# Performance work log

Measured on AMD Instinct MI355X. Metric: run time of the kernel, lower is better.

The kernel has to match this reference:

```python
import jax, jax.numpy as jnp
import numpy as np

R = 0.25
M = 0


def setup_inputs() -> dict:
    key = jax.random.key(0)
    k1, k2, k3, k4 = jax.random.split(key, 4)
    B, T_cmp, C = 2, 4096, 4096
    H, KVH, D, W = 32, 8, 128, 512
    return {
        "x_m": jax.random.normal(k1, (B, 2 * T_cmp, C), dtype=jnp.float32),
        "xm_cmp": jax.random.normal(k2, (B, T_cmp, C), dtype=jnp.float32),
        "q_w": jax.random.normal(k3, (B, H, W, D), dtype=jnp.float32),
        "km_cmp": jax.random.normal(k4, (B, KVH, T_cmp, D), dtype=jnp.float32),
    }


def reference(x_m, xm_cmp, q_w, km_cmp):
    B, T_cmp, C = xm_cmp.shape
    groups = q_w.shape[1] // km_cmp.shape[1]  # GQA repeat factor
    scaling = q_w.shape[-1] ** -0.5

    # importance_score: repeat kv heads, scaled-dot attention, softmax over keys,
    # sum over query positions, mean over heads -> [B, T_cmp]
    km = jnp.repeat(km_cmp, groups, axis=1)  # [B, H, T_cmp, D]
    scores = jnp.einsum('bhqd,bhkd->bhqk', q_w, km) * scaling
    weights = jax.nn.softmax(scores, axis=-1)
    importance = weights.sum(axis=2).mean(axis=1)  # [B, T_cmp]

    # select_indices: static top-k count
    k = min(int(R * T_cmp + M * (1 - R) / 2), T_cmp)
    _, idx = jax.lax.top_k(importance, k)  # [B, k]

    # interleave_selected: selected compressed tokens are replaced by their
    # two original tokens x_m[2t], x_m[2t+1]; others keep xm_cmp[t].
    b_idx = jnp.arange(B)[:, None]
    expand_mask = jnp.zeros((B, T_cmp), dtype=bool).at[b_idx, idx].set(True)
    sizes = jnp.where(expand_mask, 2, 1)
    start = jnp.cumsum(sizes, axis=1) - sizes  # output start position per token
    T_out = T_cmp + k

    first = jnp.where(expand_mask[..., None], x_m[:, ::2], xm_cmp)  # [B,T_cmp,C]
    second = x_m[:, 1::2]  # [B, T_cmp, C]
    pos2 = jnp.where(expand_mask, start + 1, T_out)  # non-expanded -> dummy slot

    y = jnp.zeros((B, T_out + 1, C), dtype=xm_cmp.dtype)
    y = y.at[b_idx, start].set(first)
    y = y.at[b_idx, pos2].set(second)
    return y[:, :T_out]
```

## Files before the change

kernel.cpp:

```cpp
#include <hip/hip_runtime.h>
#include <hip/hip_bf16.h>

#define B_    2
#define H_    32
#define KVH_  8
#define T_    4096
#define C_    4096
#define D_    128
#define W_    512
#define KTOP  1024
#define TOUT  (T_ + KTOP)
#define QB    64
#define NQB   (W_/QB)
#define TB    64
#define NTT   (T_/TB)
#define NPART (H_*NQB)
#define NBLK  (NQB*H_*B_)
#define SCALE 0.08838834764831845f

typedef __attribute__((ext_vector_type(8))) _Float16 half8;
typedef __attribute__((ext_vector_type(4))) float f32x4;

__device__ __forceinline__ void gload16(const void* g, void* l) {
    __builtin_amdgcn_global_load_lds(
        (const __attribute__((address_space(1))) void*)g,
        (__attribute__((address_space(3))) void*)l, 16, 0, 0);
}

__global__ __launch_bounds__(256) void convert_k_kernel(
    const float* __restrict__ km, _Float16* __restrict__ Khw,
    _Float16* __restrict__ Klw)
{
    int g = blockIdx.x*256 + threadIdx.x;
    size_t e = (size_t)g*8;
    int d0 = (int)(e & 127);
    size_t row = e >> 7;
    int t = (int)(row & (T_-1));
    size_t bk = row >> 12;
    int r = t & 63, tt = t >> 6;
    size_t off = (bk<<19) + (size_t)tt*(TB*D_) + (size_t)r*D_ + (d0 ^ ((r&7)<<3));
    float4 v0 = *(const float4*)(km + e);
    float4 v1 = *(const float4*)(km + e + 4);
    float f[8] = {v0.x,v0.y,v0.z,v0.w,v1.x,v1.y,v1.z,v1.w};
    half8 hh, hl;
#pragma unroll
    for (int i = 0; i < 8; ++i) {
        _Float16 hi = (_Float16)f[i];
        hh[i] = hi;
        hl[i] = (_Float16)(f[i] - (float)hi);
    }
    *(half8*)&Khw[off] = hh;
    *(half8*)&Klw[off] = hl;
}

#define STAGE(bufidx, tt)                                                   \
    {                                                                       \
        const _Float16* gh_ = gh0 + (size_t)(tt)*8192;                      \
        const _Float16* gl_ = gl0 + (size_t)(tt)*8192;                      \
        gload16(gh_,        &sKh[bufidx][ldsoff]);                          \
        gload16(gh_ + 2048, &sKh[bufidx][ldsoff + 2048]);                   \
        gload16(gh_ + 4096, &sKh[bufidx][ldsoff + 4096]);                   \
        gload16(gh_ + 6144, &sKh[bufidx][ldsoff + 6144]);                   \
        gload16(gl_,        &sKl[bufidx][ldsoff]);                          \
        gload16(gl_ + 2048, &sKl[bufidx][ldsoff + 2048]);                   \
        gload16(gl_ + 4096, &sKl[bufidx][ldsoff + 4096]);                   \
        gload16(gl_ + 6144, &sKl[bufidx][ldsoff + 6144]);                   \
    }

#define PIPE_HEAD(NTILES)                                                   \
    if (tt + 1 < (NTILES)) {                                                \
        STAGE(cur^1, tt+1);                                                 \
        asm volatile("s_waitcnt vmcnt(8)" ::: "memory");                    \
    } else {                                                                \
        asm volatile("s_waitcnt vmcnt(0)" ::: "memory");                    \
    }                                                                       \
    __builtin_amdgcn_s_barrier();

#define PIPE_TAIL()                                                         \
    asm volatile("" ::: "memory");                                          \
    __builtin_amdgcn_s_barrier();                                           \
    cur ^= 1;

#define TILE_MFMA(bufidx, acc)                                              \
    {                                                                       \
        const _Float16* bKh = sKh[bufidx];                                  \
        const _Float16* bKl = sKl[bufidx];                                  \
        const int rr = kg*16 + li;                                          \
        const int rx = (rr & 7) << 3;                                       \
        _Pragma("unroll")                                                   \
        for (int ks2 = 0; ks2 < 4; ++ks2) {                                 \
            const int off = rr*D_ + ((ks2*32 + lg*8) ^ rx);                 \
            half8 bh = *(const half8*)&bKh[off];                            \
            half8 bl = *(const half8*)&bKl[off];                            \
            _Pragma("unroll")                                               \
            for (int mm = 0; mm < 4; ++mm) {                                \
                acc[mm] = __builtin_amdgcn_mfma_f32_16x16x32_f16(qh[mm][ks2], bh, acc[mm], 0,0,0); \
                acc[mm] = __builtin_amdgcn_mfma_f32_16x16x32_f16(ql[mm][ks2], bh, acc[mm], 0,0,0); \
                acc[mm] = __builtin_amdgcn_mfma_f32_16x16x32_f16(qh[mm][ks2], bl, acc[mm], 0,0,0); \
            }                                                               \
        }                                                                   \
    }

__global__ __launch_bounds__(256, 2) void fused_imp_kernel(
    const float* __restrict__ q_w, const _Float16* __restrict__ Khw,
    const _Float16* __restrict__ Klw, float* __restrict__ partial)
{
    __shared__ __align__(16) _Float16 sKh[2][TB*D_];
    __shared__ __align__(16) _Float16 sKl[2][TB*D_];
    __shared__ float sL[4][QB];
    __shared__ float sR[QB];

    const int tid = threadIdx.x, wid = tid >> 6, lane = tid & 63;
    const int lg = lane >> 4, li = lane & 15;
    const int kg = wid;

    const int flat = blockIdx.x;
    const int xcd = flat & 7, m = flat >> 3;
    const int g = (m >> 5)*8 + xcd;
    const int r = m & 31;
    const int kvh = g & 7, b = g >> 3;
    const int hh = r >> 3, qb = r & 7;
    const int h = kvh*4 + hh;

    half8 qh[4][4], ql[4][4];
    {
        const float* qp0 = q_w + (((size_t)b*H_ + h)*W_ + qb*QB + li)*D_;
#pragma unroll
        for (int mm = 0; mm < 4; ++mm)
#pragma unroll
            for (int ks2 = 0; ks2 < 4; ++ks2) {
                const float* p = qp0 + mm*16*D_ + ks2*32 + lg*8;
                float4 v0 = *(const float4*)p;
                float4 v1 = *(const float4*)(p+4);
                float f[8] = {v0.x,v0.y,v0.z,v0.w,v1.x,v1.y,v1.z,v1.w};
#pragma unroll
                for (int e = 0; e < 8; ++e) {
                    _Float16 hv = (_Float16)f[e];
                    qh[mm][ks2][e] = hv;
                    ql[mm][ks2][e] = (_Float16)(f[e] - (float)hv);
                }
            }
    }

    const size_t kvoff = ((size_t)b*KVH_ + kvh) * ((size_t)T_*D_);
    const _Float16* gh0 = Khw + kvoff + (size_t)tid*8;
    const _Float16* gl0 = Klw + kvoff + (size_t)tid*8;
    const int ldsoff = tid*8;

    float lacc[4][4] = {};
    STAGE(0, 0);
    int cur = 0;
    for (int tt = 0; tt < NTT; ++tt) {
        PIPE_HEAD(NTT);
        f32x4 acc[4];
#pragma unroll
        for (int mm = 0; mm < 4; ++mm) acc[mm] = (f32x4){0.f,0.f,0.f,0.f};
        TILE_MFMA(cur, acc);
#pragma unroll
        for (int mm = 0; mm < 4; ++mm)
#pragma unroll
            for (int j = 0; j < 4; ++j)
                lacc[mm][j] += __expf(acc[mm][j]*SCALE);
        PIPE_TAIL();
    }
#pragma unroll
    for (int mm = 0; mm < 4; ++mm)
#pragma unroll
        for (int j = 0; j < 4; ++j) {
            float v = lacc[mm][j];
            v += __shfl_xor(v, 1); v += __shfl_xor(v, 2);
            v += __shfl_xor(v, 4); v += __shfl_xor(v, 8);
            if (li == 0) sL[kg][mm*16 + lg*4 + j] = v;
        }
    __syncthreads();
    if (tid < QB) {
        float l = sL[0][tid] + sL[1][tid] + sL[2][tid] + sL[3][tid];
        sR[tid] = 1.0f / l;
    }
    __syncthreads();
    float rv[4][4];
#pragma unroll
    for (int mm = 0; mm < 4; ++mm)
#pragma unroll
        for (int j = 0; j < 4; ++j)
            rv[mm][j] = sR[mm*16 + lg*4 + j];

    const size_t po = (((size_t)(h*NQB + qb))*B_ + b)*T_;
    STAGE(0, 0);
    cur = 0;
    for (int tt = 0; tt < NTT; ++tt) {
        PIPE_HEAD(NTT);
        f32x4 acc[4];
#pragma unroll
        for (int mm = 0; mm < 4; ++mm) acc[mm] = (f32x4){0.f,0.f,0.f,0.f};
        TILE_MFMA(cur, acc);
        float x = 0.f;
#pragma unroll
        for (int mm = 0; mm < 4; ++mm)
#pragma unroll
            for (int j = 0; j < 4; ++j)
                x += __expf(acc[mm][j]*SCALE)*rv[mm][j];
        x += __shfl_xor(x, 16); x += __shfl_xor(x, 32);
        if (lg == 0)
            partial[po + (size_t)tt*TB + kg*16 + li] = x;
        PIPE_TAIL();
    }
}

__global__ __launch_bounds__(256) void imp_reduce_kernel(
    const float* __restrict__ partial, float* __restrict__ imp)
{
    int gid = blockIdx.x*256 + threadIdx.x;
    int b = gid >> 12, t = gid & (T_-1);
    float s = 0.f;
    for (int i = 0; i < NPART; ++i)
        s += partial[((size_t)(i*B_ + b))*T_ + t];
    imp[gid] = s * (1.0f/H_);
}

__global__ __launch_bounds__(1024) void topk_kernel(
    const float* __restrict__ imp, int* __restrict__ mask, int* __restrict__ start)
{
    __shared__ int hist[256];
    __shared__ int sa[1024], sb[1024];
    __shared__ int sbin, srem;
    const int tid = threadIdx.x, b = blockIdx.x;
    const int i0 = 4*tid;

    unsigned key[4];
#pragma unroll
    for (int j = 0; j < 4; ++j) {
        unsigned u = __float_as_uint(imp[b*T_ + i0 + j]);
        key[j] = (u & 0x80000000u) ? ~u : (u | 0x80000000u);
    }

    unsigned prefix = 0;
    int k_rem = KTOP;
#pragma unroll
    for (int sh = 24; sh >= 0; sh -= 8) {
        unsigned hi_mask = (sh == 24) ? 0u : (0xFFFFFFFFu << (sh + 8));
        if (tid < 256) hist[tid] = 0;
        __syncthreads();
#pragma unroll
        for (int j = 0; j < 4; ++j)
            if ((key[j] & hi_mask) == prefix)
                atomicAdd(&hist[(key[j] >> sh) & 255], 1);
        __syncthreads();
        if (tid == 0) {
            int acc = 0, bin = 255;
            for (; bin > 0; --bin) {
                int hv = hist[bin];
                if (acc + hv >= k_rem) break;
                acc += hv;
            }
            sbin = bin; srem = k_rem - acc;
        }
        __syncthreads();
        prefix |= ((unsigned)sbin) << sh;
        k_rem = srem;
        __syncthreads();
    }

    int m[4], eq[4];
#pragma unroll
    for (int j = 0; j < 4; ++j) {
        m[j]  = key[j] > prefix ? 1 : 0;
        eq[j] = (key[j] == prefix) ? 1 : 0;
    }
    int e4 = eq[0]+eq[1]+eq[2]+eq[3];
    sa[tid] = e4;
    __syncthreads();
    {
        int *src = sa, *dst = sb;
        for (int off = 1; off < 1024; off <<= 1) {
            int v = src[tid];
            if (tid >= off) v += src[tid - off];
            dst[tid] = v;
            __syncthreads();
            int* t2 = src; src = dst; dst = t2;
        }
        int r = src[tid] - e4;
#pragma unroll
        for (int j = 0; j < 4; ++j) {
            if (eq[j] && r < k_rem) m[j] = 1;
            r += eq[j];
        }
    }
    __syncthreads();
    int s4 = m[0]+m[1]+m[2]+m[3];
    sa[tid] = s4;
    __syncthreads();
    int *src = sa, *dst = sb;
    for (int off = 1; off < 1024; off <<= 1) {
        int v = src[tid];
        if (tid >= off) v += src[tid - off];
        dst[tid] = v;
        __syncthreads();
        int* t2 = src; src = dst; dst = t2;
    }
    int excl = src[tid] - s4;
    start[b*T_+i0+0] = i0+0 + excl;
    start[b*T_+i0+1] = i0+1 + excl + m[0];
    start[b*T_+i0+2] = i0+2 + excl + m[0]+m[1];
    start[b*T_+i0+3] = i0+3 + excl + m[0]+m[1]+m[2];
    mask[b*T_+i0+0] = m[0]; mask[b*T_+i0+1] = m[1];
    mask[b*T_+i0+2] = m[2]; mask[b*T_+i0+3] = m[3];
}

__global__ __launch_bounds__(256) void scatter_kernel(
    const float* __restrict__ x_m, const float* __restrict__ xm_cmp,
    const int* __restrict__ mask, const int* __restrict__ start,
    float* __restrict__ out)
{
    const int t = blockIdx.x, b = blockIdx.y, tid = threadIdx.x;
    const int mk = mask[b*T_+t];
    const int st = start[b*T_+t];
    const float* s1 = mk ? (x_m + ((size_t)b*2*T_ + 2*t)*C_)
                         : (xm_cmp + ((size_t)b*T_ + t)*C_);
    float4* d1 = (float4*)(out + ((size_t)b*TOUT + st)*C_);
    const float4* s1v = (const float4*)s1;
    for (int i = tid; i < C_/4; i += 256) d1[i] = s1v[i];
    if (mk) {
        const float4* s2v = (const float4*)(x_m + ((size_t)b*2*T_ + 2*t+1)*C_);
        float4* d2 = d1 + C_/4;
        for (int i = tid; i < C_/4; i += 256) d2[i] = s2v[i];
    }
}

extern "C" void kernel_launch(void* const* d_in, const int* in_sizes, int n_in,
                              void* d_out, int out_size, void* d_ws, size_t ws_size,
                              hipStream_t stream)
{
    (void)in_sizes; (void)n_in; (void)out_size; (void)ws_size;
    const float* x_m    = (const float*)d_in[0];
    const float* xm_cmp = (const float*)d_in[1];
    const float* q_w    = (const float*)d_in[2];
    const float* km     = (const float*)d_in[3];
    float* out = (float*)d_out;

    char* ws = (char*)d_ws;
    _Float16* Khw   = (_Float16*)ws;
    _Float16* Klw   = (_Float16*)(ws + 16777216);
    float* partial  = (float*)(ws + 33554432);
    float* imp      = (float*)(ws + 41943040);
    int*   mask     = (int*)  (ws + 41975808);
    int*   start    = (int*)  (ws + 42008576);

    convert_k_kernel<<<dim3(4096), dim3(256), 0, stream>>>(km, Khw, Klw);
    fused_imp_kernel<<<dim3(NBLK), dim3(256), 0, stream>>>(q_w, Khw, Klw, partial);
    imp_reduce_kernel<<<dim3((B_*T_)/256), dim3(256), 0, stream>>>(partial, imp);
    topk_kernel<<<dim3(B_), dim3(1024), 0, stream>>>(imp, mask, start);
    scatter_kernel<<<dim3(T_, B_), dim3(256), 0, stream>>>(x_m, xm_cmp, mask, start, out);
}
```

Measured before the change: 314.7 us.

## Give each wave a private K slice in LDS and drop block barriers

The shared K tile is split into per-wave 16-row slices. Each wave now loads, via global_load_lds, only the rows it consumes, so the two s_barrier calls per tile in both passes can be removed and waves synchronise only through their own vmcnt waits. The vmcnt counts in the second pass are adjusted to account for the outstanding partial store. s_setprio is also raised around the MFMA block. Removing barriers lets waves drift apart, but it depends on each wave's own load completion being enough to guarantee LDS visibility, and the vmcnt accounting is fragile.

```diff
diff --git a/kernel.cpp b/kernel.cpp
--- a/kernel.cpp
+++ b/kernel.cpp
@@ -53,43 +53,28 @@
     *(half8*)&Klw[off] = hl;
 }
 
-#define STAGE(bufidx, tt)                                                   \
+#define STAGE_W(bufidx, tt)                                                 \
     {                                                                       \
         const _Float16* gh_ = gh0 + (size_t)(tt)*8192;                      \
         const _Float16* gl_ = gl0 + (size_t)(tt)*8192;                      \
-        gload16(gh_,        &sKh[bufidx][ldsoff]);                          \
-        gload16(gh_ + 2048, &sKh[bufidx][ldsoff + 2048]);                   \
-        gload16(gh_ + 4096, &sKh[bufidx][ldsoff + 4096]);                   \
-        gload16(gh_ + 6144, &sKh[bufidx][ldsoff + 6144]);                   \
-        gload16(gl_,        &sKl[bufidx][ldsoff]);                          \
-        gload16(gl_ + 2048, &sKl[bufidx][ldsoff + 2048]);                   \
-        gload16(gl_ + 4096, &sKl[bufidx][ldsoff + 4096]);                   \
-        gload16(gl_ + 6144, &sKl[bufidx][ldsoff + 6144]);                   \
-    }
-
-#define PIPE_HEAD(NTILES)                                                   \
-    if (tt + 1 < (NTILES)) {                                                \
-        STAGE(cur^1, tt+1);                                                 \
-        asm volatile("s_waitcnt vmcnt(8)" ::: "memory");                    \
-    } else {                                                                \
-        asm volatile("s_waitcnt vmcnt(0)" ::: "memory");                    \
-    }                                                                       \
-    __builtin_amdgcn_s_barrier();
-
-#define PIPE_TAIL()                                                         \
-    asm volatile("" ::: "memory");                                          \
-    __builtin_amdgcn_s_barrier();                                           \
-    cur ^= 1;
+        gload16(gh_,        &sKh[bufidx][wid][lane*8]);                     \
+        gload16(gh_ + 512,  &sKh[bufidx][wid][512 + lane*8]);               \
+        gload16(gh_ + 1024, &sKh[bufidx][wid][1024 + lane*8]);              \
+        gload16(gh_ + 1536, &sKh[bufidx][wid][1536 + lane*8]);              \
+        gload16(gl_,        &sKl[bufidx][wid][lane*8]);                     \
+        gload16(gl_ + 512,  &sKl[bufidx][wid][512 + lane*8]);               \
+        gload16(gl_ + 1024, &sKl[bufidx][wid][1024 + lane*8]);              \
+        gload16(gl_ + 1536, &sKl[bufidx][wid][1536 + lane*8]);              \
+    }
 
 #define TILE_MFMA(bufidx, acc)                                              \
     {                                                                       \
-        const _Float16* bKh = sKh[bufidx];                                  \
-        const _Float16* bKl = sKl[bufidx];                                  \
-        const int rr = kg*16 + li;                                          \
-        const int rx = (rr & 7) << 3;                                       \
+        const _Float16* bKh = sKh[bufidx][wid];                             \
+        const _Float16* bKl = sKl[bufidx][wid];                             \
+        __builtin_amdgcn_s_setprio(1);                                      \
         _Pragma("unroll")                                                   \
         for (int ks2 = 0; ks2 < 4; ++ks2) {                                 \
-            const int off = rr*D_ + ((ks2*32 + lg*8) ^ rx);                 \
+            const int off = li*D_ + ((ks2*32 + lg*8) ^ ((li & 7) << 3));    \
             half8 bh = *(const half8*)&bKh[off];                            \
             half8 bl = *(const half8*)&bKl[off];                            \
             _Pragma("unroll")                                               \
@@ -99,14 +84,15 @@
                 acc[mm] = __builtin_amdgcn_mfma_f32_16x16x32_f16(qh[mm][ks2], bl, acc[mm], 0,0,0); \
             }                                                               \
         }                                                                   \
+        __builtin_amdgcn_s_setprio(0);                                      \
     }
 
 __global__ __launch_bounds__(256, 2) void fused_imp_kernel(
     const float* __restrict__ q_w, const _Float16* __restrict__ Khw,
     const _Float16* __restrict__ Klw, float* __restrict__ partial)
 {
-    __shared__ __align__(16) _Float16 sKh[2][TB*D_];
-    __shared__ __align__(16) _Float16 sKl[2][TB*D_];
+    __shared__ __align__(16) _Float16 sKh[2][4][16*D_];
+    __shared__ __align__(16) _Float16 sKl[2][4][16*D_];
     __shared__ float sL[4][QB];
     __shared__ float sR[QB];
 
@@ -143,15 +129,19 @@
     }
 
     const size_t kvoff = ((size_t)b*KVH_ + kvh) * ((size_t)T_*D_);
-    const _Float16* gh0 = Khw + kvoff + (size_t)tid*8;
-    const _Float16* gl0 = Klw + kvoff + (size_t)tid*8;
-    const int ldsoff = tid*8;
+    const _Float16* gh0 = Khw + kvoff + (size_t)wid*2048 + (size_t)lane*8;
+    const _Float16* gl0 = Klw + kvoff + (size_t)wid*2048 + (size_t)lane*8;
 
     float lacc[4][4] = {};
-    STAGE(0, 0);
+    STAGE_W(0, 0);
     int cur = 0;
     for (int tt = 0; tt < NTT; ++tt) {
-        PIPE_HEAD(NTT);
+        if (tt + 1 < NTT) {
+            STAGE_W(cur^1, tt+1);
+            asm volatile("s_waitcnt vmcnt(8)" ::: "memory");
+        } else {
+            asm volatile("s_waitcnt vmcnt(0)" ::: "memory");
+        }
         f32x4 acc[4];
 #pragma unroll
         for (int mm = 0; mm < 4; ++mm) acc[mm] = (f32x4){0.f,0.f,0.f,0.f};
@@ -161,7 +151,7 @@
 #pragma unroll
             for (int j = 0; j < 4; ++j)
                 lacc[mm][j] += __expf(acc[mm][j]*SCALE);
-        PIPE_TAIL();
+        cur ^= 1;
     }
 #pragma unroll
     for (int mm = 0; mm < 4; ++mm)
@@ -186,10 +176,18 @@
             rv[mm][j] = sR[mm*16 + lg*4 + j];
 
     const size_t po = (((size_t)(h*NQB + qb))*B_ + b)*T_;
-    STAGE(0, 0);
+    STAGE_W(0, 0);
     cur = 0;
     for (int tt = 0; tt < NTT; ++tt) {
-        PIPE_HEAD(NTT);
+        if (tt == 0) {
+            STAGE_W(cur^1, 1);
+            asm volatile("s_waitcnt vmcnt(8)" ::: "memory");
+        } else if (tt + 1 < NTT) {
+            STAGE_W(cur^1, tt+1);
+            asm volatile("s_waitcnt vmcnt(9)" ::: "memory");
+        } else {
+            asm volatile("s_waitcnt vmcnt(1)" ::: "memory");
+        }
         f32x4 acc[4];
 #pragma unroll
         for (int mm = 0; mm < 4; ++mm) acc[mm] = (f32x4){0.f,0.f,0.f,0.f};
@@ -203,7 +201,7 @@
         x += __shfl_xor(x, 16); x += __shfl_xor(x, 32);
         if (lg == 0)
             partial[po + (size_t)tt*TB + kg*16 + li] = x;
-        PIPE_TAIL();
+        cur ^= 1;
     }
 }
 
```

Result: no change. 314.0 us (-0.2%).
